# Performance work log

Measured on AMD Instinct MI355X. Metric: run time of the kernel, lower is better.

## Reference

```python
import jax, jax.numpy as jnp
import numpy as np

IN_FEATURES = 4096
OUT_FEATURES = 4096
TOKENS = 8192


def setup_inputs() -> dict:
    key = jax.random.key(0)
    kx, kw, kb = jax.random.split(key, 3)
    x = jax.random.normal(kx, (TOKENS, IN_FEATURES), dtype=jnp.float32)
    # Simulate the offline quantization: a float weight quantized to 2-bit signed {-2,-1,0,1}
    w_f = jax.random.normal(kw, (OUT_FEATURES, IN_FEATURES), dtype=jnp.float32) * 0.02
    max_val = jnp.max(jnp.abs(w_f))
    scale = (max_val / 1.5 + 1e-8).astype(jnp.float32)
    weight_q = jnp.clip(jnp.round(w_f / scale), -2, 1).astype(jnp.int8)
    bias = jax.random.normal(kb, (OUT_FEATURES,), dtype=jnp.float32) * 0.01
    return {"x": x, "weight_q": weight_q, "scale": scale, "bias": bias}


def reference(x, weight_q, scale, bias):
    # Dequantize 2-bit weights then standard linear: y = x @ W^T + b
    w = weight_q.astype(jnp.float32) * scale  # [out, in]
    return jnp.einsum('ti,oi->to', x, w) + bias
```

## Files before the change

kernel.cpp:

```cpp
#include <hip/hip_runtime.h>
#include <stdint.h>

#define TOKENS 8192
#define INF    4096
#define OUTF   4096
#define NT     64

typedef __bf16 bf16x8 __attribute__((ext_vector_type(8)));
typedef float  f32x4  __attribute__((ext_vector_type(4)));
typedef unsigned short ushort_t;

__device__ __forceinline__ unsigned short f2bf(float f) {
  union { float f; unsigned int u; } v;
  v.f = f;
  unsigned int r = v.u + 0x7fffu + ((v.u >> 16) & 1u);
  return (unsigned short)(r >> 16);
}

__global__ void l2b_conv_x(const float* __restrict__ x,
                           unsigned short* __restrict__ xb, int n4) {
  int idx = blockIdx.x * blockDim.x + threadIdx.x;
  int stride = gridDim.x * blockDim.x;
  for (int i = idx; i < n4; i += stride) {
    float4 v = reinterpret_cast<const float4*>(x)[i];
    ushort4 o;
    o.x = f2bf(v.x); o.y = f2bf(v.y); o.z = f2bf(v.z); o.w = f2bf(v.w);
    reinterpret_cast<ushort4*>(xb)[i] = o;
  }
}

__global__ void l2b_conv_w(const int* __restrict__ w,
                           unsigned short* __restrict__ wb, int n4) {
  int idx = blockIdx.x * blockDim.x + threadIdx.x;
  int stride = gridDim.x * blockDim.x;
  for (int i = idx; i < n4; i += stride) {
    int4 v = reinterpret_cast<const int4*>(w)[i];
    ushort4 o;
    o.x = f2bf((float)v.x); o.y = f2bf((float)v.y);
    o.z = f2bf((float)v.z); o.w = f2bf((float)v.w);
    reinterpret_cast<ushort4*>(wb)[i] = o;
  }
}

__device__ __forceinline__ void gload_lds16(const ushort_t* g, ushort_t* l) {
  auto gp = reinterpret_cast<__attribute__((address_space(1))) unsigned int*>(
      reinterpret_cast<uintptr_t>(g));
  auto lp = reinterpret_cast<__attribute__((address_space(3))) unsigned int*>(
      reinterpret_cast<uintptr_t>(l));
  __builtin_amdgcn_global_load_lds(gp, lp, 16, 0, 0);
}

__device__ __forceinline__ int swz(int b) { return b ^ (((b >> 9) & 1) << 5); }

__device__ __forceinline__ bf16x8 ldsRd(const ushort_t* slot, int row, int colb) {
  int off = (row << 7) | colb;
  off ^= ((off >> 9) & 1) << 5;
  return *reinterpret_cast<const bf16x8*>(
      reinterpret_cast<const char*>(slot) + off);
}

__device__ __forceinline__ void stage_half(const ushort_t* __restrict__ src,
                                           ushort_t* slot, int wid,
                                           int ge0, int ge1) {
  gload_lds16(src + ge0, slot + wid * 512);
  gload_lds16(src + ge1, slot + 4096 + wid * 512);
}

__device__ __forceinline__ f32x4 mfma(bf16x8 a, bf16x8 b, f32x4 c) {
  return __builtin_amdgcn_mfma_f32_16x16x32_bf16(a, b, c, 0, 0, 0);
}

template <int N>
__device__ __forceinline__ void vmwait() {
  if constexpr (N == 4)      asm volatile("s_waitcnt vmcnt(4)" ::: "memory");
  else if constexpr (N == 0) asm volatile("s_waitcnt vmcnt(0)" ::: "memory");
}

#define PHASE_SYNC()                                            \
  __builtin_amdgcn_s_barrier();                                 \
  asm volatile("s_waitcnt lgkmcnt(0)" ::: "memory");            \
  __builtin_amdgcn_s_setprio(1)

#define PHASE_END() __builtin_amdgcn_s_setprio(0)

template <int VMB, bool STG1, bool STG2>
__device__ __forceinline__ void ktile(
    const ushort_t* __restrict__ A, const ushort_t* __restrict__ B,
    int rowBlk, int colBlk, int t,
    ushort_t* rA0, ushort_t* rA1, ushort_t* rB0, ushort_t* rB1,
    ushort_t* oA1, ushort_t* oB0,
    f32x4 (&acc)[8][4], int ar, int br, int fk, int wid, int ge0, int ge1) {
  bf16x8 a[4][2], b[2][2];
#pragma unroll
  for (int m = 0; m < 4; ++m) {
    a[m][0] = ldsRd(rA0, ar + m * 16, fk * 16);
    a[m][1] = ldsRd(rA0, ar + m * 16, 64 + fk * 16);
  }
#pragma unroll
  for (int n = 0; n < 2; ++n) {
    b[n][0] = ldsRd(rB0, br + n * 16, fk * 16);
    b[n][1] = ldsRd(rB0, br + n * 16, 64 + fk * 16);
  }
  if (STG1)
    stage_half(A + (size_t)(rowBlk + 128) * INF + (t + 1) * 64, oA1, wid, ge0, ge1);
  asm volatile("s_waitcnt lgkmcnt(8)" ::: "memory");
  PHASE_SYNC();
#pragma unroll
  for (int m = 0; m < 4; ++m)
#pragma unroll
    for (int n = 0; n < 2; ++n) {
      acc[m][n] = mfma(a[m][0], b[n][0], acc[m][n]);
      acc[m][n] = mfma(a[m][1], b[n][1], acc[m][n]);
    }
  PHASE_END();
  __builtin_amdgcn_s_barrier();
#pragma unroll
  for (int n = 0; n < 2; ++n) {
    b[n][0] = ldsRd(rB1, br + n * 16, fk * 16);
    b[n][1] = ldsRd(rB1, br + n * 16, 64 + fk * 16);
  }
  if (STG1)
    stage_half(B + (size_t)colBlk * INF + (t + 1) * 64, oB0, wid, ge0, ge1);
  PHASE_SYNC();
#pragma unroll
  for (int m = 0; m < 4; ++m)
#pragma unroll
    for (int n = 0; n < 2; ++n) {
      acc[m][2 + n] = mfma(a[m][0], b[n][0], acc[m][2 + n]);
      acc[m][2 + n] = mfma(a[m][1], b[n][1], acc[m][2 + n]);
    }
  PHASE_END();
  __builtin_amdgcn_s_barrier();
#pragma unroll
  for (int m = 0; m < 4; ++m) {
    a[m][0] = ldsRd(rA1, ar + m * 16, fk * 16);
    a[m][1] = ldsRd(rA1, ar + m * 16, 64 + fk * 16);
  }
  if (STG2)
    stage_half(A + (size_t)rowBlk * INF + (t + 2) * 64, rA0, wid, ge0, ge1);
  PHASE_SYNC();
#pragma unroll
  for (int m = 0; m < 4; ++m)
#pragma unroll
    for (int n = 0; n < 2; ++n) {
      acc[4 + m][2 + n] = mfma(a[m][0], b[n][0], acc[4 + m][2 + n]);
      acc[4 + m][2 + n] = mfma(a[m][1], b[n][1], acc[4 + m][2 + n]);
    }
  PHASE_END();
  __builtin_amdgcn_s_barrier();
#pragma unroll
  for (int n = 0; n < 2; ++n) {
    b[n][0] = ldsRd(rB0, br + n * 16, fk * 16);
    b[n][1] = ldsRd(rB0, br + n * 16, 64 + fk * 16);
  }
  if (STG2)
    stage_half(B + (size_t)(colBlk + 128) * INF + (t + 2) * 64, rB1, wid, ge0, ge1);
  PHASE_SYNC();
#pragma unroll
  for (int m = 0; m < 4; ++m)
#pragma unroll
    for (int n = 0; n < 2; ++n) {
      acc[4 + m][n] = mfma(a[m][0], b[n][0], acc[4 + m][n]);
      acc[4 + m][n] = mfma(a[m][1], b[n][1], acc[4 + m][n]);
    }
  PHASE_END();
  if (VMB >= 0) vmwait<VMB >= 0 ? VMB : 0>();
  __builtin_amdgcn_s_barrier();
}

__global__ __launch_bounds__(512, 2) void l2b_gemm8(
    const ushort_t* __restrict__ A, const ushort_t* __restrict__ B,
    const float* __restrict__ scale, const float* __restrict__ bias,
    float* __restrict__ C) {
  extern __shared__ ushort_t smem[];
  ushort_t* sA00 = smem;              ushort_t* sA01 = smem + 8192;
  ushort_t* sA10 = smem + 16384;      ushort_t* sA11 = smem + 24576;
  ushort_t* sB00 = smem + 32768;      ushort_t* sB01 = smem + 40960;
  ushort_t* sB10 = smem + 49152;      ushort_t* sB11 = smem + 57344;

  const int tid  = threadIdx.x;
  const int lane = tid & 63;
  const int wid  = tid >> 6;
  const int wm = wid >> 2, wn = wid & 3;
  const int fr = lane & 15, fk = lane >> 4;
  const int ar = wm * 64 + fr;
  const int br = wn * 32 + fr;

  const int bid = (int)blockIdx.x;
  const int idx = (bid & 7) * 64 + (bid >> 3);
  const int bm = idx >> 4, bn = idx & 15;
  const int rowBlk = bm * 256, colBlk = bn * 256;

  const int ob0 = wid * 1024 + lane * 16;
  const int ob1 = 8192 + ob0;
  const int p0 = swz(ob0), p1 = swz(ob1);
  const int ge0 = (p0 >> 7) * INF + ((p0 & 127) >> 1);
  const int ge1 = (p1 >> 7) * INF + ((p1 & 127) >> 1);

  stage_half(A + (size_t)rowBlk * INF,               sA00, wid, ge0, ge1);
  stage_half(B + (size_t)(colBlk + 128) * INF,       sB01, wid, ge0, ge1);
  stage_half(A + (size_t)(rowBlk + 128) * INF,       sA01, wid, ge0, ge1);
  stage_half(B + (size_t)colBlk * INF,               sB00, wid, ge0, ge1);
  stage_half(A + (size_t)rowBlk * INF + 64,          sA10, wid, ge0, ge1);
  stage_half(B + (size_t)(colBlk + 128) * INF + 64,  sB11, wid, ge0, ge1);
  asm volatile("s_waitcnt vmcnt(4)" ::: "memory");
  __builtin_amdgcn_s_barrier();

  f32x4 acc[8][4] = {};

#pragma unroll 1
  for (int i = 0; i < 31; ++i) {
    const int t = 2 * i;
    ktile<4, true, true>(A, B, rowBlk, colBlk, t,
        sA00, sA01, sB00, sB01, sA11, sB10,
        acc, ar, br, fk, wid, ge0, ge1);
    ktile<4, true, true>(A, B, rowBlk, colBlk, t + 1,
        sA10, sA11, sB10, sB11, sA01, sB00,
        acc, ar, br, fk, wid, ge0, ge1);
  }
  ktile<0, true, false>(A, B, rowBlk, colBlk, 62,
      sA00, sA01, sB00, sB01, sA11, sB10,
      acc, ar, br, fk, wid, ge0, ge1);
  ktile<-1, false, false>(A, B, rowBlk, colBlk, 63,
      sA10, sA11, sB10, sB11, sA01, sB00,
      acc, ar, br, fk, wid, ge0, ge1);

  const float s = scale[0];
#pragma unroll
  for (int ni = 0; ni < 4; ++ni) {
    const int nh = ni >> 1, n = ni & 1;
    const int col = colBlk + nh * 128 + wn * 32 + n * 16 + fr;
    const float bv = bias[col];
#pragma unroll
    for (int mi = 0; mi < 8; ++mi) {
      const int mh = mi >> 2, m = mi & 3;
      const int row = rowBlk + mh * 128 + wm * 64 + m * 16 + fk * 4;
#pragma unroll
      for (int j = 0; j < 4; ++j)
        C[(size_t)(row + j) * OUTF + col] = acc[mi][ni][j] * s + bv;
    }
  }
}

__global__ __launch_bounds__(256) void l2b_gemm(
    const ushort_t* __restrict__ A, const ushort_t* __restrict__ B,
    const float* __restrict__ scale, const float* __restrict__ bias,
    float* __restrict__ C) {
  constexpr int K = INF;
  constexpr int N = OUTF;
  __shared__ __align__(16) ushort_t ldsA[128 * 32];
  __shared__ __align__(16) ushort_t ldsB[128 * 32];
  const int tid = threadIdx.x;
  const int lane = tid & 63;
  const int wid = tid >> 6;
  const int wm = wid >> 1, wn = wid & 1;
  const int bm = blockIdx.x >> 5, bn = blockIdx.x & 31;
  const int row0 = bm * 128, col0 = bn * 128;
  const int lr = lane >> 4, lc = lane & 15;
  f32x4 acc[4][4] = {};
  for (int k0 = 0; k0 < K; k0 += 32) {
#pragma unroll
    for (int i = 0; i < 2; ++i) {
      const int idx = i * 256 + tid;
      const int r = idx >> 2;
      const int c = (idx & 3) * 8;
      ushort_t* lbaseA = ldsA + i * 2048 + wid * 512;
      ushort_t* lbaseB = ldsB + i * 2048 + wid * 512;
      gload_lds16(A + (size_t)(row0 + r) * K + (k0 + c), lbaseA);
      gload_lds16(B + (size_t)(col0 + r) * K + (k0 + c), lbaseB);
    }
    __syncthreads();
    bf16x8 af[4], bfr[4];
#pragma unroll
    for (int m = 0; m < 4; ++m)
      af[m] = *reinterpret_cast<const bf16x8*>(
          &ldsA[(wm * 64 + m * 16 + lc) * 32 + lr * 8]);
#pragma unroll
    for (int n = 0; n < 4; ++n)
      bfr[n] = *reinterpret_cast<const bf16x8*>(
          &ldsB[(wn * 64 + n * 16 + lc) * 32 + lr * 8]);
#pragma unroll
    for (int m = 0; m < 4; ++m)
#pragma unroll
      for (int n = 0; n < 4; ++n)
        acc[m][n] = mfma(af[m], bfr[n], acc[m][n]);
    __syncthreads();
  }
  const float s = scale[0];
#pragma unroll
  for (int n = 0; n < 4; ++n) {
    const int col = col0 + wn * 64 + n * 16 + lc;
    const float bv = bias[col];
#pragma unroll
    for (int m = 0; m < 4; ++m) {
      const int row = row0 + wm * 64 + m * 16 + lr * 4;
#pragma unroll
      for (int i = 0; i < 4; ++i)
        C[(size_t)(row + i) * N + col] = acc[m][n][i] * s + bv;
    }
  }
}

__global__ void l2b_naive(const float* __restrict__ x, const int* __restrict__ w,
                          const float* __restrict__ scale,
                          const float* __restrict__ bias,
                          float* __restrict__ out) {
  const int o = blockIdx.x * blockDim.x + threadIdx.x;
  if (o >= TOKENS * OUTF) return;
  const int t = o / OUTF;
  const int n = o - t * OUTF;
  const float* xr = x + (size_t)t * INF;
  const int* wr = w + (size_t)n * INF;
  float acc = 0.f;
  for (int k = 0; k < INF; ++k) acc += xr[k] * (float)wr[k];
  out[o] = acc * scale[0] + bias[n];
}

extern "C" void kernel_launch(void* const* d_in, const int* in_sizes, int n_in,
                              void* d_out, int out_size, void* d_ws, size_t ws_size,
                              hipStream_t stream) {
  const float* x     = (const float*)d_in[0];
  const int*   wq    = (const int*)d_in[1];
  const float* scale = (const float*)d_in[2];
  const float* bias  = (const float*)d_in[3];
  float* out = (float*)d_out;

  const size_t xbytes = (size_t)TOKENS * INF * 2;
  const size_t wbytes = (size_t)OUTF * INF * 2;

  if (ws_size >= xbytes + wbytes) {
    unsigned short* xb = (unsigned short*)d_ws;
    unsigned short* wb = (unsigned short*)((char*)d_ws + xbytes);
    l2b_conv_x<<<2048, 256, 0, stream>>>(x, xb, TOKENS * INF / 4);
    l2b_conv_w<<<2048, 256, 0, stream>>>(wq, wb, OUTF * INF / 4);

    hipError_t e = hipFuncSetAttribute(
        reinterpret_cast<const void*>(l2b_gemm8),
        hipFuncAttributeMaxDynamicSharedMemorySize, 131072);
    if (e == hipSuccess) {
      l2b_gemm8<<<dim3((TOKENS / 256) * (OUTF / 256)), 512, 131072, stream>>>(
          xb, wb, scale, bias, out);
    } else {
      l2b_gemm<<<dim3((TOKENS / 128) * (OUTF / 128)), 256, 0, stream>>>(
          xb, wb, scale, bias, out);
    }
  } else {
    l2b_naive<<<(TOKENS * OUTF + 255) / 256, 256, 0, stream>>>(
        x, wq, scale, bias, out);
  }
}
```

Before: 295.7 us.

## Switch GEMM to FP8 MX-scaled MFMA with fp8 activation and weight conversion

Activations are converted to FP8 (E4M3) rather than bf16, and the 2-bit weights map to exact FP8 codes through a lookup constant. The GEMM now uses the 16x16x128 scaled f8f6f4 MFMA with unit scales, which halves operand bytes and the number of K tiles. The existing 256x256 pipelined LDS schedule is kept, with each K tile covering 128 bytes. Quantizing activations to FP8 loses a lot of precision relative to the bf16 reference path and may break accuracy tolerances.

```diff
diff --git a/kernel.cpp b/kernel.cpp
--- a/kernel.cpp
+++ b/kernel.cpp
@@ -4,11 +4,54 @@
 #define TOKENS 8192
 #define INF    4096
 #define OUTF   4096
-#define NT     64
+#define NTQ    32
 
 typedef __bf16 bf16x8 __attribute__((ext_vector_type(8)));
 typedef float  f32x4  __attribute__((ext_vector_type(4)));
+typedef int    i32x4  __attribute__((ext_vector_type(4)));
+typedef int    i32x8  __attribute__((ext_vector_type(8)));
 typedef unsigned short ushort_t;
+typedef unsigned char  u8;
+
+#if defined(__has_builtin)
+#  if __has_builtin(__builtin_amdgcn_mfma_scale_f32_16x16x128_f8f6f4) && \
+      __has_builtin(__builtin_amdgcn_cvt_pk_fp8_f32)
+#    define HAS_MX 1
+#  else
+#    define HAS_MX 0
+#  endif
+#else
+#  define HAS_MX 0
+#endif
+
+__device__ __forceinline__ void gload_lds16(const void* g, void* l) {
+  auto gp = reinterpret_cast<__attribute__((address_space(1))) unsigned int*>(
+      reinterpret_cast<uintptr_t>(g));
+  auto lp = reinterpret_cast<__attribute__((address_space(3))) unsigned int*>(
+      reinterpret_cast<uintptr_t>(l));
+  __builtin_amdgcn_global_load_lds(gp, lp, 16, 0, 0);
+}
+
+__device__ __forceinline__ int swz(int b) { return b ^ (((b >> 9) & 1) << 5); }
+
+__device__ __forceinline__ f32x4 mfma(bf16x8 a, bf16x8 b, f32x4 c) {
+  return __builtin_amdgcn_mfma_f32_16x16x32_bf16(a, b, c, 0, 0, 0);
+}
+
+template <int N>
+__device__ __forceinline__ void vmwait() {
+  if constexpr (N == 4)      asm volatile("s_waitcnt vmcnt(4)" ::: "memory");
+  else if constexpr (N == 0) asm volatile("s_waitcnt vmcnt(0)" ::: "memory");
+}
+
+#define PHASE_SYNC()                                            \
+  __builtin_amdgcn_s_barrier();                                 \
+  asm volatile("s_waitcnt lgkmcnt(0)" ::: "memory");            \
+  __builtin_amdgcn_sched_barrier(0);                            \
+  __builtin_amdgcn_s_setprio(1)
+
+#define PHASE_END() __builtin_amdgcn_s_setprio(0)
+#define BAR() __builtin_amdgcn_s_barrier()
 
 __device__ __forceinline__ unsigned short f2bf(float f) {
   union { float f; unsigned int u; } v;
@@ -42,141 +85,146 @@
   }
 }
 
-__device__ __forceinline__ void gload_lds16(const ushort_t* g, ushort_t* l) {
-  auto gp = reinterpret_cast<__attribute__((address_space(1))) unsigned int*>(
-      reinterpret_cast<uintptr_t>(g));
-  auto lp = reinterpret_cast<__attribute__((address_space(3))) unsigned int*>(
-      reinterpret_cast<uintptr_t>(l));
-  __builtin_amdgcn_global_load_lds(gp, lp, 16, 0, 0);
-}
-
-__device__ __forceinline__ int swz(int b) { return b ^ (((b >> 9) & 1) << 5); }
-
-__device__ __forceinline__ bf16x8 ldsRd(const ushort_t* slot, int row, int colb) {
+#if HAS_MX
+__global__ void l2b_conv_x_q(const float* __restrict__ x,
+                             u8* __restrict__ xq, int n8) {
+  int idx = blockIdx.x * blockDim.x + threadIdx.x;
+  int stride = gridDim.x * blockDim.x;
+  for (int i = idx; i < n8; i += stride) {
+    float4 v0 = reinterpret_cast<const float4*>(x)[2 * i];
+    float4 v1 = reinterpret_cast<const float4*>(x)[2 * i + 1];
+    int u0 = __builtin_amdgcn_cvt_pk_fp8_f32(v0.x, v0.y, 0, false);
+    u0 = __builtin_amdgcn_cvt_pk_fp8_f32(v0.z, v0.w, u0, true);
+    int u1 = __builtin_amdgcn_cvt_pk_fp8_f32(v1.x, v1.y, 0, false);
+    u1 = __builtin_amdgcn_cvt_pk_fp8_f32(v1.z, v1.w, u1, true);
+    uint2 o; o.x = (unsigned)u0; o.y = (unsigned)u1;
+    reinterpret_cast<uint2*>(xq)[i] = o;
+  }
+}
+
+__device__ __forceinline__ unsigned w2q(int w) {
+  return (0x3800B8C0u >> (((unsigned)(w + 2)) * 8)) & 0xFFu;
+}
+
+__global__ void l2b_conv_w_q(const int* __restrict__ w,
+                             u8* __restrict__ wq, int n8) {
+  int idx = blockIdx.x * blockDim.x + threadIdx.x;
+  int stride = gridDim.x * blockDim.x;
+  for (int i = idx; i < n8; i += stride) {
+    int4 a = reinterpret_cast<const int4*>(w)[2 * i];
+    int4 b = reinterpret_cast<const int4*>(w)[2 * i + 1];
+    uint2 o;
+    o.x = w2q(a.x) | (w2q(a.y) << 8) | (w2q(a.z) << 16) | (w2q(a.w) << 24);
+    o.y = w2q(b.x) | (w2q(b.y) << 8) | (w2q(b.z) << 16) | (w2q(b.w) << 24);
+    reinterpret_cast<uint2*>(wq)[i] = o;
+  }
+}
+
+union F8 { i32x4 p[2]; i32x8 v; };
+
+__device__ __forceinline__ i32x4 ldsRdQ(const u8* slot, int row, int colb) {
   int off = (row << 7) | colb;
   off ^= ((off >> 9) & 1) << 5;
-  return *reinterpret_cast<const bf16x8*>(
-      reinterpret_cast<const char*>(slot) + off);
-}
-
-__device__ __forceinline__ void stage_half(const ushort_t* __restrict__ src,
-                                           ushort_t* slot, int wid,
-                                           int ge0, int ge1) {
-  gload_lds16(src + ge0, slot + wid * 512);
-  gload_lds16(src + ge1, slot + 4096 + wid * 512);
-}
-
-__device__ __forceinline__ f32x4 mfma(bf16x8 a, bf16x8 b, f32x4 c) {
-  return __builtin_amdgcn_mfma_f32_16x16x32_bf16(a, b, c, 0, 0, 0);
-}
-
-template <int N>
-__device__ __forceinline__ void vmwait() {
-  if constexpr (N == 4)      asm volatile("s_waitcnt vmcnt(4)" ::: "memory");
-  else if constexpr (N == 0) asm volatile("s_waitcnt vmcnt(0)" ::: "memory");
-}
-
-#define PHASE_SYNC()                                            \
-  __builtin_amdgcn_s_barrier();                                 \
-  asm volatile("s_waitcnt lgkmcnt(0)" ::: "memory");            \
-  __builtin_amdgcn_s_setprio(1)
-
-#define PHASE_END() __builtin_amdgcn_s_setprio(0)
+  return *reinterpret_cast<const i32x4*>(slot + off);
+}
+
+__device__ __forceinline__ void stage_halfQ(const u8* __restrict__ src,
+                                            u8* slot, int wid, int ge0, int ge1) {
+  gload_lds16(src + ge0, slot + wid * 1024);
+  gload_lds16(src + ge1, slot + 8192 + wid * 1024);
+}
+
+__device__ __forceinline__ f32x4 mfmaq(i32x8 a, i32x8 b, f32x4 c) {
+  return __builtin_amdgcn_mfma_scale_f32_16x16x128_f8f6f4(
+      a, b, c, 0, 0, 0, (int)0x7F7F7F7Fu, 0, (int)0x7F7F7F7Fu);
+}
 
 template <int VMB, bool STG1, bool STG2>
-__device__ __forceinline__ void ktile(
-    const ushort_t* __restrict__ A, const ushort_t* __restrict__ B,
+__device__ __forceinline__ void ktileQ(
+    const u8* __restrict__ A, const u8* __restrict__ B,
     int rowBlk, int colBlk, int t,
-    ushort_t* rA0, ushort_t* rA1, ushort_t* rB0, ushort_t* rB1,
-    ushort_t* oA1, ushort_t* oB0,
+    u8* rA0, u8* rA1, u8* rB0, u8* rB1,
+    u8* oA1, u8* oB0,
     f32x4 (&acc)[8][4], int ar, int br, int fk, int wid, int ge0, int ge1) {
-  bf16x8 a[4][2], b[2][2];
+  F8 a[4], b[2];
 #pragma unroll
   for (int m = 0; m < 4; ++m) {
-    a[m][0] = ldsRd(rA0, ar + m * 16, fk * 16);
-    a[m][1] = ldsRd(rA0, ar + m * 16, 64 + fk * 16);
+    a[m].p[0] = ldsRdQ(rA0, ar + m * 16, fk * 32);
+    a[m].p[1] = ldsRdQ(rA0, ar + m * 16, fk * 32 + 16);
   }
 #pragma unroll
   for (int n = 0; n < 2; ++n) {
-    b[n][0] = ldsRd(rB0, br + n * 16, fk * 16);
-    b[n][1] = ldsRd(rB0, br + n * 16, 64 + fk * 16);
+    b[n].p[0] = ldsRdQ(rB0, br + n * 16, fk * 32);
+    b[n].p[1] = ldsRdQ(rB0, br + n * 16, fk * 32 + 16);
   }
   if (STG1)
-    stage_half(A + (size_t)(rowBlk + 128) * INF + (t + 1) * 64, oA1, wid, ge0, ge1);
+    stage_halfQ(A + (size_t)(rowBlk + 128) * INF + (t + 1) * 128, oA1, wid, ge0, ge1);
   asm volatile("s_waitcnt lgkmcnt(8)" ::: "memory");
   PHASE_SYNC();
 #pragma unroll
   for (int m = 0; m < 4; ++m)
 #pragma unroll
-    for (int n = 0; n < 2; ++n) {
-      acc[m][n] = mfma(a[m][0], b[n][0], acc[m][n]);
-      acc[m][n] = mfma(a[m][1], b[n][1], acc[m][n]);
-    }
+    for (int n = 0; n < 2; ++n)
+      acc[m][n] = mfmaq(a[m].v, b[n].v, acc[m][n]);
   PHASE_END();
-  __builtin_amdgcn_s_barrier();
+  BAR();
 #pragma unroll
   for (int n = 0; n < 2; ++n) {
-    b[n][0] = ldsRd(rB1, br + n * 16, fk * 16);
-    b[n][1] = ldsRd(rB1, br + n * 16, 64 + fk * 16);
+    b[n].p[0] = ldsRdQ(rB1, br + n * 16, fk * 32);
+    b[n].p[1] = ldsRdQ(rB1, br + n * 16, fk * 32 + 16);
   }
   if (STG1)
-    stage_half(B + (size_t)colBlk * INF + (t + 1) * 64, oB0, wid, ge0, ge1);
+    stage_halfQ(B + (size_t)colBlk * INF + (t + 1) * 128, oB0, wid, ge0, ge1);
   PHASE_SYNC();
 #pragma unroll
   for (int m = 0; m < 4; ++m)
 #pragma unroll
-    for (int n = 0; n < 2; ++n) {
-      acc[m][2 + n] = mfma(a[m][0], b[n][0], acc[m][2 + n]);
-      acc[m][2 + n] = mfma(a[m][1], b[n][1], acc[m][2 + n]);
-    }
+    for (int n = 0; n < 2; ++n)
+      acc[m][2 + n] = mfmaq(a[m].v, b[n].v, acc[m][2 + n]);
   PHASE_END();
-  __builtin_amdgcn_s_barrier();
+  BAR();
 #pragma unroll
   for (int m = 0; m < 4; ++m) {
-    a[m][0] = ldsRd(rA1, ar + m * 16, fk * 16);
-    a[m][1] = ldsRd(rA1, ar + m * 16, 64 + fk * 16);
+    a[m].p[0] = ldsRdQ(rA1, ar + m * 16, fk * 32);
+    a[m].p[1] = ldsRdQ(rA1, ar + m * 16, fk * 32 + 16);
   }
   if (STG2)
-    stage_half(A + (size_t)rowBlk * INF + (t + 2) * 64, rA0, wid, ge0, ge1);
+    stage_halfQ(A + (size_t)rowBlk * INF + (t + 2) * 128, rA0, wid, ge0, ge1);
   PHASE_SYNC();
 #pragma unroll
   for (int m = 0; m < 4; ++m)
 #pragma unroll
-    for (int n = 0; n < 2; ++n) {
-      acc[4 + m][2 + n] = mfma(a[m][0], b[n][0], acc[4 + m][2 + n]);
-      acc[4 + m][2 + n] = mfma(a[m][1], b[n][1], acc[4 + m][2 + n]);
-    }
+    for (int n = 0; n < 2; ++n)
+      acc[4 + m][2 + n] = mfmaq(a[m].v, b[n].v, acc[4 + m][2 + n]);
   PHASE_END();
-  __builtin_amdgcn_s_barrier();
+  BAR();
 #pragma unroll
   for (int n = 0; n < 2; ++n) {
-    b[n][0] = ldsRd(rB0, br + n * 16, fk * 16);
-    b[n][1] = ldsRd(rB0, br + n * 16, 64 + fk * 16);
+    b[n].p[0] = ldsRdQ(rB0, br + n * 16, fk * 32);
+    b[n].p[1] = ldsRdQ(rB0, br + n * 16, fk * 32 + 16);
   }
   if (STG2)
-    stage_half(B + (size_t)(colBlk + 128) * INF + (t + 2) * 64, rB1, wid, ge0, ge1);
+    stage_halfQ(B + (size_t)(colBlk + 128) * INF + (t + 2) * 128, rB1, wid, ge0, ge1);
   PHASE_SYNC();
 #pragma unroll
   for (int m = 0; m < 4; ++m)
 #pragma unroll
-    for (int n = 0; n < 2; ++n) {
-      acc[4 + m][n] = mfma(a[m][0], b[n][0], acc[4 + m][n]);
-      acc[4 + m][n] = mfma(a[m][1], b[n][1], acc[4 + m][n]);
-    }
+    for (int n = 0; n < 2; ++n)
+      acc[4 + m][n] = mfmaq(a[m].v, b[n].v, acc[4 + m][n]);
   PHASE_END();
   if (VMB >= 0) vmwait<VMB >= 0 ? VMB : 0>();
-  __builtin_amdgcn_s_barrier();
-}
-
-__global__ __launch_bounds__(512, 2) void l2b_gemm8(
-    const ushort_t* __restrict__ A, const ushort_t* __restrict__ B,
+  BAR();
+}
+
+__global__ __launch_bounds__(512, 2) void l2b_gemm_mx(
+    const u8* __restrict__ A, const u8* __restrict__ B,
     const float* __restrict__ scale, const float* __restrict__ bias,
     float* __restrict__ C) {
-  extern __shared__ ushort_t smem[];
-  ushort_t* sA00 = smem;              ushort_t* sA01 = smem + 8192;
-  ushort_t* sA10 = smem + 16384;      ushort_t* sA11 = smem + 24576;
-  ushort_t* sB00 = smem + 32768;      ushort_t* sB01 = smem + 40960;
-  ushort_t* sB10 = smem + 49152;      ushort_t* sB11 = smem + 57344;
+  extern __shared__ u8 smemq[];
+  u8* sA00 = smemq;              u8* sA01 = smemq + 16384;
+  u8* sA10 = smemq + 32768;      u8* sA11 = smemq + 49152;
+  u8* sB00 = smemq + 65536;      u8* sB01 = smemq + 81920;
+  u8* sB10 = smemq + 98304;      u8* sB11 = smemq + 114688;
 
   const int tid  = threadIdx.x;
   const int lane = tid & 63;
@@ -194,34 +242,34 @@
   const int ob0 = wid * 1024 + lane * 16;
   const int ob1 = 8192 + ob0;
   const int p0 = swz(ob0), p1 = swz(ob1);
-  const int ge0 = (p0 >> 7) * INF + ((p0 & 127) >> 1);
-  const int ge1 = (p1 >> 7) * INF + ((p1 & 127) >> 1);
-
-  stage_half(A + (size_t)rowBlk * INF,               sA00, wid, ge0, ge1);
-  stage_half(B + (size_t)(colBlk + 128) * INF,       sB01, wid, ge0, ge1);
-  stage_half(A + (size_t)(rowBlk + 128) * INF,       sA01, wid, ge0, ge1);
-  stage_half(B + (size_t)colBlk * INF,               sB00, wid, ge0, ge1);
-  stage_half(A + (size_t)rowBlk * INF + 64,          sA10, wid, ge0, ge1);
-  stage_half(B + (size_t)(colBlk + 128) * INF + 64,  sB11, wid, ge0, ge1);
+  const int ge0 = (p0 >> 7) * INF + (p0 & 127);
+  const int ge1 = (p1 >> 7) * INF + (p1 & 127);
+
+  stage_halfQ(A + (size_t)rowBlk * INF,               sA00, wid, ge0, ge1);
+  stage_halfQ(B + (size_t)(colBlk + 128) * INF,       sB01, wid, ge0, ge1);
+  stage_halfQ(A + (size_t)(rowBlk + 128) * INF,       sA01, wid, ge0, ge1);
+  stage_halfQ(B + (size_t)colBlk * INF,               sB00, wid, ge0, ge1);
+  stage_halfQ(A + (size_t)rowBlk * INF + 128,         sA10, wid, ge0, ge1);
+  stage_halfQ(B + (size_t)(colBlk + 128) * INF + 128, sB11, wid, ge0, ge1);
   asm volatile("s_waitcnt vmcnt(4)" ::: "memory");
-  __builtin_amdgcn_s_barrier();
+  BAR();
 
   f32x4 acc[8][4] = {};
 
 #pragma unroll 1
-  for (int i = 0; i < 31; ++i) {
+  for (int i = 0; i < (NTQ - 2) / 2; ++i) {
     const int t = 2 * i;
-    ktile<4, true, true>(A, B, rowBlk, colBlk, t,
+    ktileQ<4, true, true>(A, B, rowBlk, colBlk, t,
         sA00, sA01, sB00, sB01, sA11, sB10,
         acc, ar, br, fk, wid, ge0, ge1);
-    ktile<4, true, true>(A, B, rowBlk, colBlk, t + 1,
+    ktileQ<4, true, true>(A, B, rowBlk, colBlk, t + 1,
         sA10, sA11, sB10, sB11, sA01, sB00,
         acc, ar, br, fk, wid, ge0, ge1);
   }
-  ktile<0, true, false>(A, B, rowBlk, colBlk, 62,
+  ktileQ<0, true, false>(A, B, rowBlk, colBlk, NTQ - 2,
       sA00, sA01, sB00, sB01, sA11, sB10,
       acc, ar, br, fk, wid, ge0, ge1);
-  ktile<-1, false, false>(A, B, rowBlk, colBlk, 63,
+  ktileQ<-1, false, false>(A, B, rowBlk, colBlk, NTQ - 1,
       sA10, sA11, sB10, sB11, sA01, sB00,
       acc, ar, br, fk, wid, ge0, ge1);
 
@@ -241,6 +289,7 @@
     }
   }
 }
+#endif
 
 __global__ __launch_bounds__(256) void l2b_gemm(
     const ushort_t* __restrict__ A, const ushort_t* __restrict__ B,
@@ -325,25 +374,34 @@
   const float* bias  = (const float*)d_in[3];
   float* out = (float*)d_out;
 
+#if HAS_MX
+  const size_t xq_bytes = (size_t)TOKENS * INF;
+  const size_t wq_bytes = (size_t)OUTF * INF;
+  if (ws_size >= xq_bytes + wq_bytes) {
+    u8* xq = (u8*)d_ws;
+    u8* wq8 = xq + xq_bytes;
+    hipError_t e = hipFuncSetAttribute(
+        reinterpret_cast<const void*>(l2b_gemm_mx),
+        hipFuncAttributeMaxDynamicSharedMemorySize, 131072);
+    if (e == hipSuccess) {
+      l2b_conv_x_q<<<2048, 256, 0, stream>>>(x, xq, TOKENS * INF / 8);
+      l2b_conv_w_q<<<2048, 256, 0, stream>>>(wq, wq8, OUTF * INF / 8);
+      l2b_gemm_mx<<<dim3((TOKENS / 256) * (OUTF / 256)), 512, 131072, stream>>>(
+          xq, wq8, scale, bias, out);
+      return;
+    }
+  }
+#endif
+
   const size_t xbytes = (size_t)TOKENS * INF * 2;
   const size_t wbytes = (size_t)OUTF * INF * 2;
-
   if (ws_size >= xbytes + wbytes) {
     unsigned short* xb = (unsigned short*)d_ws;
     unsigned short* wb = (unsigned short*)((char*)d_ws + xbytes);
     l2b_conv_x<<<2048, 256, 0, stream>>>(x, xb, TOKENS * INF / 4);
     l2b_conv_w<<<2048, 256, 0, stream>>>(wq, wb, OUTF * INF / 4);
-
-    hipError_t e = hipFuncSetAttribute(
-        reinterpret_cast<const void*>(l2b_gemm8),
-        hipFuncAttributeMaxDynamicSharedMemorySize, 131072);
-    if (e == hipSuccess) {
-      l2b_gemm8<<<dim3((TOKENS / 256) * (OUTF / 256)), 512, 131072, stream>>>(
-          xb, wb, scale, bias, out);
-    } else {
-      l2b_gemm<<<dim3((TOKENS / 128) * (OUTF / 128)), 256, 0, stream>>>(
-          xb, wb, scale, bias, out);
-    }
+    l2b_gemm<<<dim3((TOKENS / 128) * (OUTF / 128)), 256, 0, stream>>>(
+        xb, wb, scale, bias, out);
   } else {
     l2b_naive<<<(TOKENS * OUTF + 255) / 256, 256, 0, stream>>>(
         x, wq, scale, bias, out);
```

Result: slower. 351.1 us (+18.7%).

## Halve per-tile workgroup barriers by merging A/B staging and double-buffering B fragments

Applied to the files above, without the earlier changes.

Each k-tile now issues the next A and B half-tile global-to-LDS copies together, and keeps two register sets for B fragments. This lets the second and fourth MFMA phases start after only an LDS wait, so the workgroup barriers per k-tile drop from eight to four. Scheduling barriers are added so the compiler does not move LDS reads across the priority/phase boundaries. The cost is more live VGPRs for the second B fragment set. There is also a risk of LDS hazards if any wave is still reading a buffer that another wave begins overwriting.

```diff
diff --git a/kernel.cpp b/kernel.cpp
--- a/kernel.cpp
+++ b/kernel.cpp
@@ -79,9 +79,16 @@
 #define PHASE_SYNC()                                            \
   __builtin_amdgcn_s_barrier();                                 \
   asm volatile("s_waitcnt lgkmcnt(0)" ::: "memory");            \
+  __builtin_amdgcn_sched_barrier(0);                            \
   __builtin_amdgcn_s_setprio(1)
 
+#define MID_SYNC()                                              \
+  asm volatile("s_waitcnt lgkmcnt(0)" ::: "memory");            \
+  __builtin_amdgcn_sched_barrier(0);                            \
+  __builtin_amdgcn_s_setprio(1)
+
 #define PHASE_END() __builtin_amdgcn_s_setprio(0)
+#define BAR() __builtin_amdgcn_s_barrier()
 
 template <int VMB, bool STG1, bool STG2>
 __device__ __forceinline__ void ktile(
@@ -90,7 +97,7 @@
     ushort_t* rA0, ushort_t* rA1, ushort_t* rB0, ushort_t* rB1,
     ushort_t* oA1, ushort_t* oB0,
     f32x4 (&acc)[8][4], int ar, int br, int fk, int wid, int ge0, int ge1) {
-  bf16x8 a[4][2], b[2][2];
+  bf16x8 a[4][2], b0[2][2], b1[2][2];
 #pragma unroll
   for (int m = 0; m < 4; ++m) {
     a[m][0] = ldsRd(rA0, ar + m * 16, fk * 16);
@@ -98,74 +105,72 @@
   }
 #pragma unroll
   for (int n = 0; n < 2; ++n) {
-    b[n][0] = ldsRd(rB0, br + n * 16, fk * 16);
-    b[n][1] = ldsRd(rB0, br + n * 16, 64 + fk * 16);
-  }
-  if (STG1)
+    b0[n][0] = ldsRd(rB0, br + n * 16, fk * 16);
+    b0[n][1] = ldsRd(rB0, br + n * 16, 64 + fk * 16);
+  }
+  if (STG1) {
     stage_half(A + (size_t)(rowBlk + 128) * INF + (t + 1) * 64, oA1, wid, ge0, ge1);
+    stage_half(B + (size_t)colBlk * INF + (t + 1) * 64, oB0, wid, ge0, ge1);
+  }
   asm volatile("s_waitcnt lgkmcnt(8)" ::: "memory");
   PHASE_SYNC();
 #pragma unroll
   for (int m = 0; m < 4; ++m)
 #pragma unroll
     for (int n = 0; n < 2; ++n) {
-      acc[m][n] = mfma(a[m][0], b[n][0], acc[m][n]);
-      acc[m][n] = mfma(a[m][1], b[n][1], acc[m][n]);
+      acc[m][n] = mfma(a[m][0], b0[n][0], acc[m][n]);
+      acc[m][n] = mfma(a[m][1], b0[n][1], acc[m][n]);
     }
   PHASE_END();
-  __builtin_amdgcn_s_barrier();
 #pragma unroll
   for (int n = 0; n < 2; ++n) {
-    b[n][0] = ldsRd(rB1, br + n * 16, fk * 16);
-    b[n][1] = ldsRd(rB1, br + n * 16, 64 + fk * 16);
-  }
-  if (STG1)
-    stage_half(B + (size_t)colBlk * INF + (t + 1) * 64, oB0, wid, ge0, ge1);
-  PHASE_SYNC();
+    b1[n][0] = ldsRd(rB1, br + n * 16, fk * 16);
+    b1[n][1] = ldsRd(rB1, br + n * 16, 64 + fk * 16);
+  }
+  MID_SYNC();
 #pragma unroll
   for (int m = 0; m < 4; ++m)
 #pragma unroll
     for (int n = 0; n < 2; ++n) {
-      acc[m][2 + n] = mfma(a[m][0], b[n][0], acc[m][2 + n]);
-      acc[m][2 + n] = mfma(a[m][1], b[n][1], acc[m][2 + n]);
+      acc[m][2 + n] = mfma(a[m][0], b1[n][0], acc[m][2 + n]);
+      acc[m][2 + n] = mfma(a[m][1], b1[n][1], acc[m][2 + n]);
     }
   PHASE_END();
-  __builtin_amdgcn_s_barrier();
+  BAR();
 #pragma unroll
   for (int m = 0; m < 4; ++m) {
     a[m][0] = ldsRd(rA1, ar + m * 16, fk * 16);
     a[m][1] = ldsRd(rA1, ar + m * 16, 64 + fk * 16);
   }
-  if (STG2)
+  if (STG2) {
     stage_half(A + (size_t)rowBlk * INF + (t + 2) * 64, rA0, wid, ge0, ge1);
+    stage_half(B + (size_t)(colBlk + 128) * INF + (t + 2) * 64, rB1, wid, ge0, ge1);
+  }
   PHASE_SYNC();
 #pragma unroll
   for (int m = 0; m < 4; ++m)
 #pragma unroll
     for (int n = 0; n < 2; ++n) {
-      acc[4 + m][2 + n] = mfma(a[m][0], b[n][0], acc[4 + m][2 + n]);
-      acc[4 + m][2 + n] = mfma(a[m][1], b[n][1], acc[4 + m][2 + n]);
+      acc[4 + m][2 + n] = mfma(a[m][0], b1[n][0], acc[4 + m][2 + n]);
+      acc[4 + m][2 + n] = mfma(a[m][1], b1[n][1], acc[4 + m][2 + n]);
     }
   PHASE_END();
-  __builtin_amdgcn_s_barrier();
 #pragma unroll
   for (int n = 0; n < 2; ++n) {
-    b[n][0] = ldsRd(rB0, br + n * 16, fk * 16);
-    b[n][1] = ldsRd(rB0, br + n * 16, 64 + fk * 16);
-  }
-  if (STG2)
-    stage_half(B + (size_t)(colBlk + 128) * INF + (t + 2) * 64, rB1, wid, ge0, ge1);
-  PHASE_SYNC();
+    b0[n][0] = ldsRd(rB0, br + n * 16, fk * 16);
+    b0[n][1] = ldsRd(rB0, br + n * 16, 64 + fk * 16);
+  }
+  MID_SYNC();
 #pragma unroll
   for (int m = 0; m < 4; ++m)
 #pragma unroll
     for (int n = 0; n < 2; ++n) {
-      acc[4 + m][n] = mfma(a[m][0], b[n][0], acc[4 + m][n]);
-      acc[4 + m][n] = mfma(a[m][1], b[n][1], acc[4 + m][n]);
+      acc[4 + m][n] = mfma(a[m][0], b0[n][0], acc[4 + m][n]);
+      acc[4 + m][n] = mfma(a[m][1], b0[n][1], acc[4 + m][n]);
     }
   PHASE_END();
   if (VMB >= 0) vmwait<VMB >= 0 ? VMB : 0>();
-  __builtin_amdgcn_s_barrier();
+  BAR();
 }
 
 __global__ __launch_bounds__(512, 2) void l2b_gemm8(
```

Result: no change. 297.0 us (+0.4%).
